# Kernel tuning notes

Hardware: AMD Instinct MI355X
Metric: run time of the kernel (lower is better)

## Reference

```python
import jax, jax.numpy as jnp
import numpy as np

D_MODEL = 1024
D_KEY = 64
N_HEADS = 16
B, T = 4, 2048


def setup_inputs() -> dict:
    key = jax.random.key(0)
    ks = jax.random.split(key, 12)
    s = 0.02
    return {
        "keys": jax.random.normal(ks[0], (B, T, D_MODEL), jnp.float32),
        "queries": jax.random.normal(ks[1], (B, T, D_MODEL), jnp.float32),
        "values": jax.random.normal(ks[2], (B, T, D_MODEL), jnp.float32),
        "pad_mask": jnp.ones((B, T), jnp.int32),
        "WK_w": jax.random.normal(ks[3], (D_KEY * N_HEADS, D_MODEL), jnp.float32) * s,
        "WK_b": jnp.zeros((D_KEY * N_HEADS,), jnp.float32),
        "WQ_w": jax.random.normal(ks[4], (D_KEY * N_HEADS, D_MODEL), jnp.float32) * s,
        "WQ_b": jnp.zeros((D_KEY * N_HEADS,), jnp.float32),
        "WV_w": jax.random.normal(ks[5], (D_KEY * N_HEADS, D_MODEL), jnp.float32) * s,
        "WV_b": jnp.zeros((D_KEY * N_HEADS,), jnp.float32),
        "WO_w": jax.random.normal(ks[6], (D_MODEL, D_KEY * N_HEADS), jnp.float32) * s,
        "WO_b": jnp.zeros((D_MODEL,), jnp.float32),
    }


def reference(keys, queries, values, pad_mask, WK_w, WK_b, WQ_w, WQ_b, WV_w, WV_b, WO_w, WO_b):
    # NOTE: the original torch module calls masked_fill (non-inplace) and discards
    # the result, so neither the causal mask nor pad_mask has any effect. We
    # faithfully reproduce that: no masking. pad_mask is an unused constant.
    batch, time = keys.shape[:2]
    k = keys @ WK_w.T + WK_b      # [B,T,H*dk]
    q = queries @ WQ_w.T + WQ_b
    v = values @ WV_w.T + WV_b

    def split_heads(x):
        return x.reshape(batch, time, N_HEADS, D_KEY).transpose(0, 2, 1, 3)  # [B,H,T,dk]

    k, q, v = split_heads(k), split_heads(q), split_heads(v)
    # scores[t,s] = k_t . q_s / sqrt(d_key)  (K and Q swapped, as in source)
    scores = jnp.einsum("bhtd,bhsd->bhts", k, q) / jnp.sqrt(jnp.float32(D_KEY))
    attn = jax.nn.softmax(scores, axis=-1)             # [B,H,T,T]
    ctx = jnp.einsum("bhts,bhsd->bhtd", attn, v)       # [B,H,T,dk]
    ctx = ctx.transpose(0, 2, 1, 3).reshape(batch, time, N_HEADS * D_KEY)
    return ctx @ WO_w.T + WO_b
```

## Files before the change

kernel.cpp:

```cpp
#include <hip/hip_runtime.h>

typedef unsigned short u16;
typedef unsigned int u32;
typedef __attribute__((ext_vector_type(8))) short short8;
typedef __attribute__((ext_vector_type(4))) float f32x4;

__device__ __forceinline__ u16 f2bf(float f) {
    unsigned int u = __float_as_uint(f);
    u += 0x7fffu + ((u >> 16) & 1u);
    return (u16)(u >> 16);
}

__device__ __forceinline__ u32 pack_trunc(float a, float b) {
    return __builtin_amdgcn_perm(__float_as_uint(b), __float_as_uint(a), 0x07060302u);
}

__device__ __forceinline__ void gload16(const u16* g, const u16* l) {
    __builtin_amdgcn_global_load_lds(
        (const __attribute__((address_space(1))) unsigned int*)g,
        (__attribute__((address_space(3))) unsigned int*)l, 16, 0, 0);
}

__global__ __launch_bounds__(256) void cast_all(const float* __restrict__ k,
                                                const float* __restrict__ q,
                                                const float* __restrict__ v,
                                                const float* __restrict__ wk,
                                                const float* __restrict__ wq,
                                                const float* __restrict__ wv,
                                                const float* __restrict__ wo,
                                                u16* __restrict__ Xk, u16* __restrict__ Xq,
                                                u16* __restrict__ Xv, u16* __restrict__ Wk,
                                                u16* __restrict__ Wq, u16* __restrict__ Wv,
                                                u16* __restrict__ Wo) {
    size_t i = ((size_t)blockIdx.x * 256 + threadIdx.x) * 8;
    const float* src; u16* dst; size_t off;
    if (i < 25165824) {
        int r = (int)(i >> 23); off = i & 8388607;
        src = r == 0 ? k : (r == 1 ? q : v);
        dst = r == 0 ? Xk : (r == 1 ? Xq : Xv);
    } else {
        size_t j = i - 25165824;
        int r = (int)(j >> 20); off = j & 1048575;
        src = r == 0 ? wk : (r == 1 ? wq : (r == 2 ? wv : wo));
        dst = r == 0 ? Wk : (r == 1 ? Wq : (r == 2 ? Wv : Wo));
    }
    float4 a = *(const float4*)(src + off);
    float4 b = *(const float4*)(src + off + 4);
    union { u16 h[8]; uint4 u; } r8;
    r8.h[0] = f2bf(a.x); r8.h[1] = f2bf(a.y); r8.h[2] = f2bf(a.z); r8.h[3] = f2bf(a.w);
    r8.h[4] = f2bf(b.x); r8.h[5] = f2bf(b.y); r8.h[6] = f2bf(b.z); r8.h[7] = f2bf(b.w);
    *(uint4*)(dst + off) = r8.u;
}

__global__ __launch_bounds__(256) void gemm_qkv(const u16* __restrict__ Xk,
                                                const u16* __restrict__ Xq,
                                                const u16* __restrict__ Xv,
                                                const u16* __restrict__ Wk,
                                                const u16* __restrict__ Wq,
                                                const u16* __restrict__ Wv,
                                                const float* __restrict__ bK,
                                                const float* __restrict__ bQ,
                                                const float* __restrict__ bV,
                                                u16* __restrict__ Kbh,
                                                u16* __restrict__ Qbh,
                                                u16* __restrict__ Vtg,
                                                float kscale) {
    __shared__ u16 sA[128 * 32];
    __shared__ u16 sB[128 * 32];
    const int f = blockIdx.x;
    const int z = f >> 9;
    const int r9 = f & 511;
    const int i_idx = (r9 & 7) | (((r9 >> 6) & 7) << 3);
    const int j_idx = (r9 >> 3) & 7;

    const u16* X = z == 0 ? Xk : (z == 1 ? Xq : Xv);
    const u16* W = z == 0 ? Wk : (z == 1 ? Wq : Wv);
    const float* bias = z == 0 ? bK : (z == 1 ? bQ : bV);
    u16* out = z == 0 ? Kbh : (z == 1 ? Qbh : Vtg);
    const float scale = z == 0 ? kscale : 1.0f;

    const int tid  = threadIdx.x;
    const int wave = tid >> 6, lane = tid & 63;
    const int quad = lane >> 4, l16 = lane & 15;
    const int wm = wave & 1, wn = wave >> 1;
    const int i0 = i_idx * 128, j0 = j_idx * 128;
    const int lrow = tid >> 2, lseg = tid & 3;

    f32x4 acc[4][4];
    #pragma unroll
    for (int mt = 0; mt < 4; mt++)
        #pragma unroll
        for (int nt = 0; nt < 4; nt++) acc[mt][nt] = (f32x4){0.f, 0.f, 0.f, 0.f};

    const u16* gA0 = X + (size_t)(i0 + lrow) * 1024 + lseg * 8;
    const u16* gA1 = X + (size_t)(i0 + 64 + lrow) * 1024 + lseg * 8;
    const u16* gB0 = W + (size_t)(j0 + lrow) * 1024 + lseg * 8;
    const u16* gB1 = W + (size_t)(j0 + 64 + lrow) * 1024 + lseg * 8;
    const u16* lA0 = sA + wave * 512;
    const u16* lA1 = sA + 2048 + wave * 512;
    const u16* lB0 = sB + wave * 512;
    const u16* lB1 = sB + 2048 + wave * 512;

    for (int kk = 0; kk < 1024; kk += 32) {
        __syncthreads();
        gload16(gA0 + kk, lA0);
        gload16(gA1 + kk, lA1);
        gload16(gB0 + kk, lB0);
        gload16(gB1 + kk, lB1);
        __syncthreads();
        short8 af[4], bf[4];
        #pragma unroll
        for (int mt = 0; mt < 4; mt++)
            af[mt] = *(const short8*)&sA[(wm * 64 + mt * 16 + l16) * 32 + quad * 8];
        #pragma unroll
        for (int nt = 0; nt < 4; nt++)
            bf[nt] = *(const short8*)&sB[(wn * 64 + nt * 16 + l16) * 32 + quad * 8];
        #pragma unroll
        for (int mt = 0; mt < 4; mt++)
            #pragma unroll
            for (int nt = 0; nt < 4; nt++)
                acc[mt][nt] = __builtin_amdgcn_mfma_f32_16x16x32_bf16(af[mt], bf[nt], acc[mt][nt], 0, 0, 0);
    }

    #pragma unroll
    for (int mt = 0; mt < 4; mt++) {
        #pragma unroll
        for (int nt = 0; nt < 4; nt++) {
            int j = j0 + wn * 64 + nt * 16 + l16;
            float bj = bias[j];
            #pragma unroll
            for (int r = 0; r < 4; r++) {
                int i = i0 + wm * 64 + mt * 16 + quad * 4 + r;
                float v = (acc[mt][nt][r] + bj) * scale;
                int b = i >> 11, t = i & 2047;
                int h = j >> 6,  dd = j & 63;
                size_t idx;
                if (z == 2) idx = (((size_t)(b * 16 + h)) * 64 + dd) * 2048 + t;
                else        idx = (((size_t)(b * 16 + h)) * 2048 + t) * 64 + dd;
                out[idx] = f2bf(v);
            }
        }
    }
}

__global__ __launch_bounds__(256) void gemm_out(const u16* __restrict__ X,
                                                const u16* __restrict__ W,
                                                const float* __restrict__ bias,
                                                float* __restrict__ out) {
    __shared__ u16 sA[128 * 32];
    __shared__ u16 sB[64 * 32];
    const int f = blockIdx.x;
    const int j_idx = (f >> 3) & 15;
    const int i_idx = (f & 7) | ((f >> 7) << 3);
    const int tid  = threadIdx.x;
    const int wave = tid >> 6, lane = tid & 63;
    const int quad = lane >> 4, l16 = lane & 15;
    const int wm = wave & 1, wn = wave >> 1;
    const int i0 = i_idx * 128, j0 = j_idx * 64;
    const int lrow = tid >> 2, lseg = tid & 3;

    f32x4 acc[4][2];
    #pragma unroll
    for (int mt = 0; mt < 4; mt++) {
        acc[mt][0] = (f32x4){0.f, 0.f, 0.f, 0.f};
        acc[mt][1] = (f32x4){0.f, 0.f, 0.f, 0.f};
    }

    const u16* gA0 = X + (size_t)(i0 + lrow) * 1024 + lseg * 8;
    const u16* gA1 = X + (size_t)(i0 + 64 + lrow) * 1024 + lseg * 8;
    const u16* gB0 = W + (size_t)(j0 + lrow) * 1024 + lseg * 8;
    const u16* lA0 = sA + wave * 512;
    const u16* lA1 = sA + 2048 + wave * 512;
    const u16* lB0 = sB + wave * 512;

    for (int kk = 0; kk < 1024; kk += 32) {
        __syncthreads();
        gload16(gA0 + kk, lA0);
        gload16(gA1 + kk, lA1);
        gload16(gB0 + kk, lB0);
        __syncthreads();
        short8 af[4], bf[2];
        #pragma unroll
        for (int mt = 0; mt < 4; mt++)
            af[mt] = *(const short8*)&sA[(wm * 64 + mt * 16 + l16) * 32 + quad * 8];
        #pragma unroll
        for (int nt = 0; nt < 2; nt++)
            bf[nt] = *(const short8*)&sB[(wn * 32 + nt * 16 + l16) * 32 + quad * 8];
        #pragma unroll
        for (int mt = 0; mt < 4; mt++)
            #pragma unroll
            for (int nt = 0; nt < 2; nt++)
                acc[mt][nt] = __builtin_amdgcn_mfma_f32_16x16x32_bf16(af[mt], bf[nt], acc[mt][nt], 0, 0, 0);
    }

    #pragma unroll
    for (int mt = 0; mt < 4; mt++) {
        #pragma unroll
        for (int nt = 0; nt < 2; nt++) {
            int j = j0 + wn * 32 + nt * 16 + l16;
            float bj = bias[j];
            #pragma unroll
            for (int r = 0; r < 4; r++) {
                int i = i0 + wm * 64 + mt * 16 + quad * 4 + r;
                out[(size_t)i * 1024 + j] = acc[mt][nt][r] + bj;
            }
        }
    }
}

#define QST 72

__global__ __launch_bounds__(256, 2) void attn_kernel(const u16* __restrict__ Kbh,
                                                      const u16* __restrict__ Qbh,
                                                      const u16* __restrict__ Vtg,
                                                      u16* __restrict__ ctx) {
    __shared__ u16 sQ[64 * QST];
    __shared__ u16 sVt[64 * QST];
    __shared__ u16 sP[4 * 2 * 16 * QST];
    const int f = blockIdx.x;
    const int bh = (f & 7) | ((f >> 6) << 3);
    const int tx = (f >> 3) & 7;
    const int tid  = threadIdx.x;
    const int wave = tid >> 6, lane = tid & 63;
    const int quad = lane >> 4, l16 = lane & 15;
    const int t0 = tx * 256;
    const int tw = t0 + wave * 64;
    const size_t base = (size_t)bh * 2048 * 64;

    short8 bk[4][2];
    #pragma unroll
    for (int g = 0; g < 4; g++) {
        const u16* kr = Kbh + base + (size_t)(tw + g * 16 + l16) * 64 + quad * 8;
        bk[g][0] = *(const short8*)kr;
        bk[g][1] = *(const short8*)(kr + 32);
    }
    const short8 ones = {0x3F80, 0x3F80, 0x3F80, 0x3F80, 0x3F80, 0x3F80, 0x3F80, 0x3F80};

    f32x4 accO[4][4];
    #pragma unroll
    for (int g = 0; g < 4; g++)
        #pragma unroll
        for (int dt = 0; dt < 4; dt++) accO[g][dt] = (f32x4){0.f, 0.f, 0.f, 0.f};
    f32x4 accL[4];
    #pragma unroll
    for (int g = 0; g < 4; g++) accL[g] = (f32x4){0.f, 0.f, 0.f, 0.f};

    const int srow = tid >> 2, seg = tid & 3;
    u16* sPw = sP + wave * 2 * 16 * QST;

    for (int s0 = 0; s0 < 2048; s0 += 64) {
        __syncthreads();
        {
            const uint4* gq = (const uint4*)(Qbh + base + (size_t)(s0 + srow) * 64 + seg * 16);
            uint4 q0 = gq[0], q1 = gq[1];
            *(uint4*)&sQ[srow * QST + seg * 16]     = q0;
            *(uint4*)&sQ[srow * QST + seg * 16 + 8] = q1;
        }
        {
            const uint4* gv = (const uint4*)(Vtg + ((size_t)bh * 64 + srow) * 2048 + s0 + seg * 16);
            uint4 v0 = gv[0], v1 = gv[1];
            *(uint4*)&sVt[srow * QST + seg * 16]     = v0;
            *(uint4*)&sVt[srow * QST + seg * 16 + 8] = v1;
        }
        __syncthreads();

        short8 aq[4][2], av[2][4];
        #pragma unroll
        for (int nt = 0; nt < 4; nt++) {
            aq[nt][0] = *(const short8*)&sQ[(nt * 16 + l16) * QST + quad * 8];
            aq[nt][1] = *(const short8*)&sQ[(nt * 16 + l16) * QST + 32 + quad * 8];
        }
        #pragma unroll
        for (int kk = 0; kk < 2; kk++)
            #pragma unroll
            for (int dt = 0; dt < 4; dt++)
                av[kk][dt] = *(const short8*)&sVt[(dt * 16 + l16) * QST + kk * 32 + quad * 8];

        #pragma unroll
        for (int g = 0; g < 4; g++) {
            f32x4 aS[4];
            #pragma unroll
            for (int nt = 0; nt < 4; nt++) {
                f32x4 s = __builtin_amdgcn_mfma_f32_16x16x32_bf16(aq[nt][0], bk[g][0],
                            (f32x4){0.f, 0.f, 0.f, 0.f}, 0, 0, 0);
                aS[nt] = __builtin_amdgcn_mfma_f32_16x16x32_bf16(aq[nt][1], bk[g][1], s, 0, 0, 0);
            }
            u16* pb = sPw + (g & 1) * 16 * QST;
            #pragma unroll
            for (int nt = 0; nt < 4; nt++) {
                float p0 = __builtin_amdgcn_exp2f(aS[nt][0]);
                float p1 = __builtin_amdgcn_exp2f(aS[nt][1]);
                float p2 = __builtin_amdgcn_exp2f(aS[nt][2]);
                float p3 = __builtin_amdgcn_exp2f(aS[nt][3]);
                uint2 pk = { pack_trunc(p0, p1), pack_trunc(p2, p3) };
                *(uint2*)&pb[l16 * QST + nt * 16 + quad * 4] = pk;
            }
            #pragma unroll
            for (int kk = 0; kk < 2; kk++) {
                short8 bp = *(const short8*)&pb[l16 * QST + kk * 32 + quad * 8];
                accL[g] = __builtin_amdgcn_mfma_f32_16x16x32_bf16(ones, bp, accL[g], 0, 0, 0);
                #pragma unroll
                for (int dt = 0; dt < 4; dt++)
                    accO[g][dt] = __builtin_amdgcn_mfma_f32_16x16x32_bf16(av[kk][dt], bp, accO[g][dt], 0, 0, 0);
            }
        }
    }

    const int b = bh >> 4, h = bh & 15;
    #pragma unroll
    for (int g = 0; g < 4; g++) {
        float inv = 1.f / accL[g][0];
        int t = tw + g * 16 + l16;
        u16* orow = ctx + ((size_t)(b * 2048 + t)) * 1024 + h * 64;
        #pragma unroll
        for (int dt = 0; dt < 4; dt++) {
            union { u16 h4[4]; uint2 u; } o;
            #pragma unroll
            for (int r = 0; r < 4; r++) o.h4[r] = f2bf(accO[g][dt][r] * inv);
            *(uint2*)&orow[dt * 16 + quad * 4] = o.u;
        }
    }
}

extern "C" void kernel_launch(void* const* d_in, const int* in_sizes, int n_in,
                              void* d_out, int out_size, void* d_ws, size_t ws_size,
                              hipStream_t stream) {
    const float* keys    = (const float*)d_in[0];
    const float* queries = (const float*)d_in[1];
    const float* values  = (const float*)d_in[2];
    const float* WKb = (const float*)d_in[5];
    const float* WQb = (const float*)d_in[7];
    const float* WVb = (const float*)d_in[9];
    const float* WOb = (const float*)d_in[11];

    char* ws = (char*)d_ws;
    const size_t MB = 1 << 20;
    u16* Kbh = (u16*)(ws + 0 * MB);
    u16* Qbh = (u16*)(ws + 16 * MB);
    u16* Vtg = (u16*)(ws + 32 * MB);
    u16* Xk  = (u16*)(ws + 48 * MB);
    u16* Xq  = (u16*)(ws + 64 * MB);
    u16* Xv  = (u16*)(ws + 80 * MB);
    u16* Wk  = (u16*)(ws + 96 * MB);
    u16* Wq  = (u16*)(ws + 98 * MB);
    u16* Wv  = (u16*)(ws + 100 * MB);
    u16* Wo  = (u16*)(ws + 102 * MB);
    u16* ctx = (u16*)(ws + 48 * MB);

    cast_all<<<14336, 256, 0, stream>>>(keys, queries, values,
                                        (const float*)d_in[4], (const float*)d_in[6],
                                        (const float*)d_in[8], (const float*)d_in[10],
                                        Xk, Xq, Xv, Wk, Wq, Wv, Wo);

    const float kscale = 1.4426950408889634f * 0.125f;
    gemm_qkv<<<1536, 256, 0, stream>>>(Xk, Xq, Xv, Wk, Wq, Wv,
                                       WKb, WQb, WVb, Kbh, Qbh, Vtg, kscale);

    attn_kernel<<<512, 256, 0, stream>>>(Kbh, Qbh, Vtg, ctx);

    gemm_out<<<1024, 256, 0, stream>>>(ctx, Wo, WOb, (float*)d_out);
}
```

Measured before the change: 346.4 us.

## Double-buffer LDS tiles and swizzle layout in projection GEMMs

Both projection GEMM kernels now use two LDS buffers, so the next k-slice is loaded while the current one feeds MFMA. This removes one of the two barriers per iteration. The 16-byte chunk position within each LDS row is also XOR-swizzled by row bits, with matching swizzled reads, to reduce bank conflicts on fragment loads. LDS use doubles, which may lower occupancy, and overlap depends on how the compiler places the waitcnt before the barrier.

```diff
diff --git a/kernel.cpp b/kernel.cpp
--- a/kernel.cpp
+++ b/kernel.cpp
@@ -65,8 +65,8 @@
                                                 u16* __restrict__ Qbh,
                                                 u16* __restrict__ Vtg,
                                                 float kscale) {
-    __shared__ u16 sA[128 * 32];
-    __shared__ u16 sB[128 * 32];
+    __shared__ u16 sA[2 * 128 * 32];
+    __shared__ u16 sB[2 * 128 * 32];
     const int f = blockIdx.x;
     const int z = f >> 9;
     const int r9 = f & 511;
@@ -84,7 +84,9 @@
     const int quad = lane >> 4, l16 = lane & 15;
     const int wm = wave & 1, wn = wave >> 1;
     const int i0 = i_idx * 128, j0 = j_idx * 128;
-    const int lrow = tid >> 2, lseg = tid & 3;
+    const int lrow = tid >> 2;
+    const int lseg = (tid & 3) ^ ((tid >> 3) & 3);
+    const int sw   = (l16 >> 1) & 3;
 
     f32x4 acc[4][4];
     #pragma unroll
@@ -96,30 +98,38 @@
     const u16* gA1 = X + (size_t)(i0 + 64 + lrow) * 1024 + lseg * 8;
     const u16* gB0 = W + (size_t)(j0 + lrow) * 1024 + lseg * 8;
     const u16* gB1 = W + (size_t)(j0 + 64 + lrow) * 1024 + lseg * 8;
-    const u16* lA0 = sA + wave * 512;
-    const u16* lA1 = sA + 2048 + wave * 512;
-    const u16* lB0 = sB + wave * 512;
-    const u16* lB1 = sB + 2048 + wave * 512;
+
+    auto stage = [&](int buf, int kk) {
+        const u16* a = sA + buf * 4096 + wave * 512;
+        const u16* b = sB + buf * 4096 + wave * 512;
+        gload16(gA0 + kk, a);
+        gload16(gA1 + kk, a + 2048);
+        gload16(gB0 + kk, b);
+        gload16(gB1 + kk, b + 2048);
+    };
+
+    stage(0, 0);
+    __syncthreads();
+    int cur = 0;
 
     for (int kk = 0; kk < 1024; kk += 32) {
-        __syncthreads();
-        gload16(gA0 + kk, lA0);
-        gload16(gA1 + kk, lA1);
-        gload16(gB0 + kk, lB0);
-        gload16(gB1 + kk, lB1);
-        __syncthreads();
+        if (kk + 32 < 1024) stage(cur ^ 1, kk + 32);
+        const u16* bA = sA + cur * 4096;
+        const u16* bB = sB + cur * 4096;
         short8 af[4], bf[4];
         #pragma unroll
         for (int mt = 0; mt < 4; mt++)
-            af[mt] = *(const short8*)&sA[(wm * 64 + mt * 16 + l16) * 32 + quad * 8];
+            af[mt] = *(const short8*)&bA[(wm * 64 + mt * 16 + l16) * 32 + (quad ^ sw) * 8];
         #pragma unroll
         for (int nt = 0; nt < 4; nt++)
-            bf[nt] = *(const short8*)&sB[(wn * 64 + nt * 16 + l16) * 32 + quad * 8];
+            bf[nt] = *(const short8*)&bB[(wn * 64 + nt * 16 + l16) * 32 + (quad ^ sw) * 8];
         #pragma unroll
         for (int mt = 0; mt < 4; mt++)
             #pragma unroll
             for (int nt = 0; nt < 4; nt++)
                 acc[mt][nt] = __builtin_amdgcn_mfma_f32_16x16x32_bf16(af[mt], bf[nt], acc[mt][nt], 0, 0, 0);
+        __syncthreads();
+        cur ^= 1;
     }
 
     #pragma unroll
@@ -147,8 +157,8 @@
                                                 const u16* __restrict__ W,
                                                 const float* __restrict__ bias,
                                                 float* __restrict__ out) {
-    __shared__ u16 sA[128 * 32];
-    __shared__ u16 sB[64 * 32];
+    __shared__ u16 sA[2 * 128 * 32];
+    __shared__ u16 sB[2 * 64 * 32];
     const int f = blockIdx.x;
     const int j_idx = (f >> 3) & 15;
     const int i_idx = (f & 7) | ((f >> 7) << 3);
@@ -157,7 +167,9 @@
     const int quad = lane >> 4, l16 = lane & 15;
     const int wm = wave & 1, wn = wave >> 1;
     const int i0 = i_idx * 128, j0 = j_idx * 64;
-    const int lrow = tid >> 2, lseg = tid & 3;
+    const int lrow = tid >> 2;
+    const int lseg = (tid & 3) ^ ((tid >> 3) & 3);
+    const int sw   = (l16 >> 1) & 3;
 
     f32x4 acc[4][2];
     #pragma unroll
@@ -169,28 +181,37 @@
     const u16* gA0 = X + (size_t)(i0 + lrow) * 1024 + lseg * 8;
     const u16* gA1 = X + (size_t)(i0 + 64 + lrow) * 1024 + lseg * 8;
     const u16* gB0 = W + (size_t)(j0 + lrow) * 1024 + lseg * 8;
-    const u16* lA0 = sA + wave * 512;
-    const u16* lA1 = sA + 2048 + wave * 512;
-    const u16* lB0 = sB + wave * 512;
+
+    auto stage = [&](int buf, int kk) {
+        const u16* a = sA + buf * 4096 + wave * 512;
+        const u16* b = sB + buf * 2048 + wave * 512;
+        gload16(gA0 + kk, a);
+        gload16(gA1 + kk, a + 2048);
+        gload16(gB0 + kk, b);
+    };
+
+    stage(0, 0);
+    __syncthreads();
+    int cur = 0;
 
     for (int kk = 0; kk < 1024; kk += 32) {
-        __syncthreads();
-        gload16(gA0 + kk, lA0);
-        gload16(gA1 + kk, lA1);
-        gload16(gB0 + kk, lB0);
-        __syncthreads();
+        if (kk + 32 < 1024) stage(cur ^ 1, kk + 32);
+        const u16* bA = sA + cur * 4096;
+        const u16* bB = sB + cur * 2048;
         short8 af[4], bf[2];
         #pragma unroll
         for (int mt = 0; mt < 4; mt++)
-            af[mt] = *(const short8*)&sA[(wm * 64 + mt * 16 + l16) * 32 + quad * 8];
+            af[mt] = *(const short8*)&bA[(wm * 64 + mt * 16 + l16) * 32 + (quad ^ sw) * 8];
         #pragma unroll
         for (int nt = 0; nt < 2; nt++)
-            bf[nt] = *(const short8*)&sB[(wn * 32 + nt * 16 + l16) * 32 + quad * 8];
+            bf[nt] = *(const short8*)&bB[(wn * 32 + nt * 16 + l16) * 32 + (quad ^ sw) * 8];
         #pragma unroll
         for (int mt = 0; mt < 4; mt++)
             #pragma unroll
             for (int nt = 0; nt < 2; nt++)
                 acc[mt][nt] = __builtin_amdgcn_mfma_f32_16x16x32_bf16(af[mt], bf[nt], acc[mt][nt], 0, 0, 0);
+        __syncthreads();
+        cur ^= 1;
     }
 
     #pragma unroll
```

Result: slower. 362.6 us (+4.7%).

## Rewrite projection GEMMs with 256x128 tiles, triple-buffered LDS and swizzle

Applied to the files above, without the earlier changes.

Both the QKV and output projection GEMMs now use 512-thread blocks computing 256x128 tiles with a K-step of 64. A three-stage LDS ring (144 KB of dynamic shared memory) lets global-to-LDS loads for future tiles overlap MFMA work, and an XOR swizzle on the LDS layout avoids bank conflicts. The block index remapping is meant to improve L2 locality. In exchange, LDS use is high enough to limit occupancy, and gemm_out launches only 256 blocks, which may underfill the GPU's compute units.

```diff
diff --git a/kernel.cpp b/kernel.cpp
--- a/kernel.cpp
+++ b/kernel.cpp
@@ -52,26 +52,107 @@
     *(uint4*)(dst + off) = r8.u;
 }
 
-__global__ __launch_bounds__(256) void gemm_qkv(const u16* __restrict__ Xk,
-                                                const u16* __restrict__ Xq,
-                                                const u16* __restrict__ Xv,
-                                                const u16* __restrict__ Wk,
-                                                const u16* __restrict__ Wq,
-                                                const u16* __restrict__ Wv,
-                                                const float* __restrict__ bK,
-                                                const float* __restrict__ bQ,
-                                                const float* __restrict__ bV,
-                                                u16* __restrict__ Kbh,
-                                                u16* __restrict__ Qbh,
-                                                u16* __restrict__ Vtg,
-                                                float kscale) {
-    __shared__ u16 sA[128 * 32];
-    __shared__ u16 sB[128 * 32];
-    const int f = blockIdx.x;
-    const int z = f >> 9;
-    const int r9 = f & 511;
-    const int i_idx = (r9 & 7) | (((r9 >> 6) & 7) << 3);
-    const int j_idx = (r9 >> 3) & 7;
+
+__device__ __forceinline__ void stage_tile(const u16* __restrict__ X, const u16* __restrict__ W,
+                                           int i0, int j0, int kt, u16* sA, u16* sB,
+                                           int tid, int wave) {
+    const int r = tid >> 3;
+    const int sg = (tid & 7) ^ (r & 7);
+    const u16* gA = X + (size_t)(i0 + r) * 1024 + kt + sg * 8;
+    const u16* gB = W + (size_t)(j0 + r) * 1024 + kt + sg * 8;
+    const u16* dA = sA + wave * 512;
+    const u16* dB = sB + wave * 512;
+    gload16(gA,               dA);
+    gload16(gA + 64 * 1024,   dA + 4096);
+    gload16(gA + 128 * 1024,  dA + 8192);
+    gload16(gA + 192 * 1024,  dA + 12288);
+    gload16(gB,               dB);
+    gload16(gB + 64 * 1024,   dB + 4096);
+}
+
+__device__ __forceinline__ void tile_mfma(const u16* sA, const u16* sB,
+                                          f32x4 (&acc)[8][2],
+                                          int wm, int wn, int quad, int l16) {
+    const int sx = l16 & 7;
+    short8 bf[2][2];
+    #pragma unroll
+    for (int nf = 0; nf < 2; nf++)
+        #pragma unroll
+        for (int kh = 0; kh < 2; kh++) {
+            int row = wn * 32 + nf * 16 + l16;
+            int slot = (quad + kh * 4) ^ sx;
+            bf[nf][kh] = *(const short8*)&sB[row * 64 + slot * 8];
+        }
+    #pragma unroll
+    for (int mh = 0; mh < 2; mh++) {
+        short8 af[4][2];
+        #pragma unroll
+        for (int mf = 0; mf < 4; mf++)
+            #pragma unroll
+            for (int kh = 0; kh < 2; kh++) {
+                int row = wm * 128 + mh * 64 + mf * 16 + l16;
+                int slot = (quad + kh * 4) ^ sx;
+                af[mf][kh] = *(const short8*)&sA[row * 64 + slot * 8];
+            }
+        #pragma unroll
+        for (int mf = 0; mf < 4; mf++)
+            #pragma unroll
+            for (int nf = 0; nf < 2; nf++)
+                #pragma unroll
+                for (int kh = 0; kh < 2; kh++)
+                    acc[mh * 4 + mf][nf] = __builtin_amdgcn_mfma_f32_16x16x32_bf16(
+                        af[mf][kh], bf[nf][kh], acc[mh * 4 + mf][nf], 0, 0, 0);
+    }
+}
+
+#define GEMM_PIPELINE(X, W)                                                              \
+    stage_tile(X, W, i0, j0, 0,  sAr,         sBr,        tid, wave);                    \
+    stage_tile(X, W, i0, j0, 64, sAr + 16384, sBr + 8192, tid, wave);                    \
+    int rs = 0;                                                                          \
+    _Pragma("unroll 1")                                                                  \
+    for (int t = 0; t < 14; t++) {                                                       \
+        asm volatile("s_waitcnt vmcnt(6)" ::: "memory");                                 \
+        __builtin_amdgcn_s_barrier();                                                    \
+        __builtin_amdgcn_s_setprio(1);                                                   \
+        tile_mfma(sAr + rs * 16384, sBr + rs * 8192, acc, wm, wn, quad, l16);            \
+        __builtin_amdgcn_s_setprio(0);                                                   \
+        __builtin_amdgcn_s_barrier();                                                    \
+        int ss = rs + 2; if (ss >= 3) ss -= 3;                                           \
+        stage_tile(X, W, i0, j0, (t + 2) * 64, sAr + ss * 16384, sBr + ss * 8192,        \
+                   tid, wave);                                                           \
+        rs = (rs == 2) ? 0 : rs + 1;                                                     \
+    }                                                                                    \
+    asm volatile("s_waitcnt vmcnt(6)" ::: "memory");             \
+    __builtin_amdgcn_s_barrier();                                                        \
+    tile_mfma(sAr + rs * 16384, sBr + rs * 8192, acc, wm, wn, quad, l16);                \
+    __builtin_amdgcn_s_barrier();                                                        \
+    rs = (rs == 2) ? 0 : rs + 1;                                                         \
+    asm volatile("s_waitcnt vmcnt(0)" ::: "memory");                     \
+    __builtin_amdgcn_s_barrier();                                                        \
+    tile_mfma(sAr + rs * 16384, sBr + rs * 8192, acc, wm, wn, quad, l16);
+
+__global__ __launch_bounds__(512, 2) void gemm_qkv(const u16* __restrict__ Xk,
+                                                   const u16* __restrict__ Xq,
+                                                   const u16* __restrict__ Xv,
+                                                   const u16* __restrict__ Wk,
+                                                   const u16* __restrict__ Wq,
+                                                   const u16* __restrict__ Wv,
+                                                   const float* __restrict__ bK,
+                                                   const float* __restrict__ bQ,
+                                                   const float* __restrict__ bV,
+                                                   u16* __restrict__ Kbh,
+                                                   u16* __restrict__ Qbh,
+                                                   u16* __restrict__ Vtg,
+                                                   float kscale) {
+    extern __shared__ __align__(16) u16 smem[];
+    u16* sAr = smem;
+    u16* sBr = smem + 49152;
+    const int f  = blockIdx.x;
+    const int wg = (f & 7) * 96 + (f >> 3);
+    const int z  = wg >> 8;
+    const int r8 = wg & 255;
+    const int i0 = (r8 >> 3) * 256;
+    const int j0 = (r8 & 7) * 128;
 
     const u16* X = z == 0 ? Xk : (z == 1 ? Xq : Xv);
     const u16* W = z == 0 ? Wk : (z == 1 ? Wq : Wv);
@@ -82,127 +163,74 @@
     const int tid  = threadIdx.x;
     const int wave = tid >> 6, lane = tid & 63;
     const int quad = lane >> 4, l16 = lane & 15;
-    const int wm = wave & 1, wn = wave >> 1;
-    const int i0 = i_idx * 128, j0 = j_idx * 128;
-    const int lrow = tid >> 2, lseg = tid & 3;
-
-    f32x4 acc[4][4];
-    #pragma unroll
-    for (int mt = 0; mt < 4; mt++)
-        #pragma unroll
-        for (int nt = 0; nt < 4; nt++) acc[mt][nt] = (f32x4){0.f, 0.f, 0.f, 0.f};
-
-    const u16* gA0 = X + (size_t)(i0 + lrow) * 1024 + lseg * 8;
-    const u16* gA1 = X + (size_t)(i0 + 64 + lrow) * 1024 + lseg * 8;
-    const u16* gB0 = W + (size_t)(j0 + lrow) * 1024 + lseg * 8;
-    const u16* gB1 = W + (size_t)(j0 + 64 + lrow) * 1024 + lseg * 8;
-    const u16* lA0 = sA + wave * 512;
-    const u16* lA1 = sA + 2048 + wave * 512;
-    const u16* lB0 = sB + wave * 512;
-    const u16* lB1 = sB + 2048 + wave * 512;
-
-    for (int kk = 0; kk < 1024; kk += 32) {
-        __syncthreads();
-        gload16(gA0 + kk, lA0);
-        gload16(gA1 + kk, lA1);
-        gload16(gB0 + kk, lB0);
-        gload16(gB1 + kk, lB1);
-        __syncthreads();
-        short8 af[4], bf[4];
-        #pragma unroll
-        for (int mt = 0; mt < 4; mt++)
-            af[mt] = *(const short8*)&sA[(wm * 64 + mt * 16 + l16) * 32 + quad * 8];
-        #pragma unroll
-        for (int nt = 0; nt < 4; nt++)
-            bf[nt] = *(const short8*)&sB[(wn * 64 + nt * 16 + l16) * 32 + quad * 8];
-        #pragma unroll
-        for (int mt = 0; mt < 4; mt++)
-            #pragma unroll
-            for (int nt = 0; nt < 4; nt++)
-                acc[mt][nt] = __builtin_amdgcn_mfma_f32_16x16x32_bf16(af[mt], bf[nt], acc[mt][nt], 0, 0, 0);
-    }
-
-    #pragma unroll
-    for (int mt = 0; mt < 4; mt++) {
-        #pragma unroll
-        for (int nt = 0; nt < 4; nt++) {
-            int j = j0 + wn * 64 + nt * 16 + l16;
+    const int wm = wave >> 2, wn = wave & 3;
+
+    f32x4 acc[8][2];
+    #pragma unroll
+    for (int m = 0; m < 8; m++) {
+        acc[m][0] = (f32x4){0.f, 0.f, 0.f, 0.f};
+        acc[m][1] = (f32x4){0.f, 0.f, 0.f, 0.f};
+    }
+
+    GEMM_PIPELINE(X, W)
+
+    #pragma unroll
+    for (int m = 0; m < 8; m++) {
+        #pragma unroll
+        for (int nf = 0; nf < 2; nf++) {
+            int j = j0 + wn * 32 + nf * 16 + l16;
             float bj = bias[j];
             #pragma unroll
             for (int r = 0; r < 4; r++) {
-                int i = i0 + wm * 64 + mt * 16 + quad * 4 + r;
-                float v = (acc[mt][nt][r] + bj) * scale;
-                int b = i >> 11, t = i & 2047;
+                int i = i0 + wm * 128 + m * 16 + quad * 4 + r;
+                float v = (acc[m][nf][r] + bj) * scale;
+                int b = i >> 11, tt = i & 2047;
                 int h = j >> 6,  dd = j & 63;
                 size_t idx;
-                if (z == 2) idx = (((size_t)(b * 16 + h)) * 64 + dd) * 2048 + t;
-                else        idx = (((size_t)(b * 16 + h)) * 2048 + t) * 64 + dd;
+                if (z == 2) idx = (((size_t)(b * 16 + h)) * 64 + dd) * 2048 + tt;
+                else        idx = (((size_t)(b * 16 + h)) * 2048 + tt) * 64 + dd;
                 out[idx] = f2bf(v);
             }
         }
     }
 }
 
-__global__ __launch_bounds__(256) void gemm_out(const u16* __restrict__ X,
-                                                const u16* __restrict__ W,
-                                                const float* __restrict__ bias,
-                                                float* __restrict__ out) {
-    __shared__ u16 sA[128 * 32];
-    __shared__ u16 sB[64 * 32];
-    const int f = blockIdx.x;
-    const int j_idx = (f >> 3) & 15;
-    const int i_idx = (f & 7) | ((f >> 7) << 3);
+__global__ __launch_bounds__(512, 2) void gemm_out(const u16* __restrict__ X,
+                                                   const u16* __restrict__ W,
+                                                   const float* __restrict__ bias,
+                                                   float* __restrict__ out) {
+    extern __shared__ __align__(16) u16 smem[];
+    u16* sAr = smem;
+    u16* sBr = smem + 49152;
+    const int f  = blockIdx.x;
+    const int wg = (f & 7) * 32 + (f >> 3);
+    const int i0 = (wg >> 3) * 256;
+    const int j0 = (wg & 7) * 128;
+
     const int tid  = threadIdx.x;
     const int wave = tid >> 6, lane = tid & 63;
     const int quad = lane >> 4, l16 = lane & 15;
-    const int wm = wave & 1, wn = wave >> 1;
-    const int i0 = i_idx * 128, j0 = j_idx * 64;
-    const int lrow = tid >> 2, lseg = tid & 3;
-
-    f32x4 acc[4][2];
-    #pragma unroll
-    for (int mt = 0; mt < 4; mt++) {
-        acc[mt][0] = (f32x4){0.f, 0.f, 0.f, 0.f};
-        acc[mt][1] = (f32x4){0.f, 0.f, 0.f, 0.f};
-    }
-
-    const u16* gA0 = X + (size_t)(i0 + lrow) * 1024 + lseg * 8;
-    const u16* gA1 = X + (size_t)(i0 + 64 + lrow) * 1024 + lseg * 8;
-    const u16* gB0 = W + (size_t)(j0 + lrow) * 1024 + lseg * 8;
-    const u16* lA0 = sA + wave * 512;
-    const u16* lA1 = sA + 2048 + wave * 512;
-    const u16* lB0 = sB + wave * 512;
-
-    for (int kk = 0; kk < 1024; kk += 32) {
-        __syncthreads();
-        gload16(gA0 + kk, lA0);
-        gload16(gA1 + kk, lA1);
-        gload16(gB0 + kk, lB0);
-        __syncthreads();
-        short8 af[4], bf[2];
-        #pragma unroll
-        for (int mt = 0; mt < 4; mt++)
-            af[mt] = *(const short8*)&sA[(wm * 64 + mt * 16 + l16) * 32 + quad * 8];
-        #pragma unroll
-        for (int nt = 0; nt < 2; nt++)
-            bf[nt] = *(const short8*)&sB[(wn * 32 + nt * 16 + l16) * 32 + quad * 8];
-        #pragma unroll
-        for (int mt = 0; mt < 4; mt++)
-            #pragma unroll
-            for (int nt = 0; nt < 2; nt++)
-                acc[mt][nt] = __builtin_amdgcn_mfma_f32_16x16x32_bf16(af[mt], bf[nt], acc[mt][nt], 0, 0, 0);
-    }
-
-    #pragma unroll
-    for (int mt = 0; mt < 4; mt++) {
-        #pragma unroll
-        for (int nt = 0; nt < 2; nt++) {
-            int j = j0 + wn * 32 + nt * 16 + l16;
+    const int wm = wave >> 2, wn = wave & 3;
+
+    f32x4 acc[8][2];
+    #pragma unroll
+    for (int m = 0; m < 8; m++) {
+        acc[m][0] = (f32x4){0.f, 0.f, 0.f, 0.f};
+        acc[m][1] = (f32x4){0.f, 0.f, 0.f, 0.f};
+    }
+
+    GEMM_PIPELINE(X, W)
+
+    #pragma unroll
+    for (int m = 0; m < 8; m++) {
+        #pragma unroll
+        for (int nf = 0; nf < 2; nf++) {
+            int j = j0 + wn * 32 + nf * 16 + l16;
             float bj = bias[j];
             #pragma unroll
             for (int r = 0; r < 4; r++) {
-                int i = i0 + wm * 64 + mt * 16 + quad * 4 + r;
-                out[(size_t)i * 1024 + j] = acc[mt][nt][r] + bj;
+                int i = i0 + wm * 128 + m * 16 + quad * 4 + r;
+                out[(size_t)i * 1024 + j] = acc[m][nf][r] + bj;
             }
         }
     }
@@ -347,16 +375,25 @@
     u16* Wo  = (u16*)(ws + 102 * MB);
     u16* ctx = (u16*)(ws + 48 * MB);
 
+    static bool attr_done = false;
+    if (!attr_done) {
+        hipFuncSetAttribute((const void*)gemm_qkv,
+                            hipFuncAttributeMaxDynamicSharedMemorySize, 147456);
+        hipFuncSetAttribute((const void*)gemm_out,
+                            hipFuncAttributeMaxDynamicSharedMemorySize, 147456);
+        attr_done = true;
+    }
+
     cast_all<<<14336, 256, 0, stream>>>(keys, queries, values,
                                         (const float*)d_in[4], (const float*)d_in[6],
                                         (const float*)d_in[8], (const float*)d_in[10],
                                         Xk, Xq, Xv, Wk, Wq, Wv, Wo);
 
     const float kscale = 1.4426950408889634f * 0.125f;
-    gemm_qkv<<<1536, 256, 0, stream>>>(Xk, Xq, Xv, Wk, Wq, Wv,
-                                       WKb, WQb, WVb, Kbh, Qbh, Vtg, kscale);
+    gemm_qkv<<<768, 512, 147456, stream>>>(Xk, Xq, Xv, Wk, Wq, Wv,
+                                           WKb, WQb, WVb, Kbh, Qbh, Vtg, kscale);
 
     attn_kernel<<<512, 256, 0, stream>>>(Kbh, Qbh, Vtg, ctx);
 
-    gemm_out<<<1024, 256, 0, stream>>>(ctx, Wo, WOb, (float*)d_out);
-}
+    gemm_out<<<256, 512, 147456, stream>>>(ctx, Wo, WOb, (float*)d_out);
+}
```

Measured after the change: 358.3 us. +3.4%, slower.

## Double GEMM K-tile to 64 and XOR-swizzle LDS layout in projection kernels

Applied to the files above, without the earlier changes.

Both the QKV and output projection GEMMs now stage a 64-wide K slice per iteration instead of 32, halving the number of barrier pairs and load rounds across the K loop. The LDS tile is stored with an XOR swizzle on 16-byte segments (applied on the global source side, since global_load_lds writes contiguously), so fragment reads from 64-element rows avoid bank conflicts. This doubles LDS use per block, which may reduce occupancy, and there is still no double buffering.

```diff
diff --git a/kernel.cpp b/kernel.cpp
--- a/kernel.cpp
+++ b/kernel.cpp
@@ -52,6 +52,7 @@
     *(uint4*)(dst + off) = r8.u;
 }
 
+
 __global__ __launch_bounds__(256) void gemm_qkv(const u16* __restrict__ Xk,
                                                 const u16* __restrict__ Xq,
                                                 const u16* __restrict__ Xv,
@@ -65,8 +66,8 @@
                                                 u16* __restrict__ Qbh,
                                                 u16* __restrict__ Vtg,
                                                 float kscale) {
-    __shared__ u16 sA[128 * 32];
-    __shared__ u16 sB[128 * 32];
+    __shared__ u16 sA[128 * 64];
+    __shared__ u16 sB[128 * 64];
     const int f = blockIdx.x;
     const int z = f >> 9;
     const int r9 = f & 511;
@@ -84,7 +85,14 @@
     const int quad = lane >> 4, l16 = lane & 15;
     const int wm = wave & 1, wn = wave >> 1;
     const int i0 = i_idx * 128, j0 = j_idx * 128;
-    const int lrow = tid >> 2, lseg = tid & 3;
+
+    const int r = tid >> 3;
+    const int sg = (tid & 7) ^ (r & 7);
+    const u16* gA = X + (size_t)(i0 + r) * 1024 + sg * 8;
+    const u16* gB = W + (size_t)(j0 + r) * 1024 + sg * 8;
+    u16* dA = sA + wave * 512;
+    u16* dB = sB + wave * 512;
+    const int sx = l16 & 7;
 
     f32x4 acc[4][4];
     #pragma unroll
@@ -92,34 +100,35 @@
         #pragma unroll
         for (int nt = 0; nt < 4; nt++) acc[mt][nt] = (f32x4){0.f, 0.f, 0.f, 0.f};
 
-    const u16* gA0 = X + (size_t)(i0 + lrow) * 1024 + lseg * 8;
-    const u16* gA1 = X + (size_t)(i0 + 64 + lrow) * 1024 + lseg * 8;
-    const u16* gB0 = W + (size_t)(j0 + lrow) * 1024 + lseg * 8;
-    const u16* gB1 = W + (size_t)(j0 + 64 + lrow) * 1024 + lseg * 8;
-    const u16* lA0 = sA + wave * 512;
-    const u16* lA1 = sA + 2048 + wave * 512;
-    const u16* lB0 = sB + wave * 512;
-    const u16* lB1 = sB + 2048 + wave * 512;
-
-    for (int kk = 0; kk < 1024; kk += 32) {
-        __syncthreads();
-        gload16(gA0 + kk, lA0);
-        gload16(gA1 + kk, lA1);
-        gload16(gB0 + kk, lB0);
-        gload16(gB1 + kk, lB1);
-        __syncthreads();
-        short8 af[4], bf[4];
-        #pragma unroll
-        for (int mt = 0; mt < 4; mt++)
-            af[mt] = *(const short8*)&sA[(wm * 64 + mt * 16 + l16) * 32 + quad * 8];
+    for (int kk = 0; kk < 1024; kk += 64) {
+        __syncthreads();
+        gload16(gA + kk,         dA);
+        gload16(gA + kk + 32768, dA + 2048);
+        gload16(gA + kk + 65536, dA + 4096);
+        gload16(gA + kk + 98304, dA + 6144);
+        gload16(gB + kk,         dB);
+        gload16(gB + kk + 32768, dB + 2048);
+        gload16(gB + kk + 65536, dB + 4096);
+        gload16(gB + kk + 98304, dB + 6144);
+        __syncthreads();
+        short8 bf[4][2];
         #pragma unroll
         for (int nt = 0; nt < 4; nt++)
-            bf[nt] = *(const short8*)&sB[(wn * 64 + nt * 16 + l16) * 32 + quad * 8];
-        #pragma unroll
-        for (int mt = 0; mt < 4; mt++)
-            #pragma unroll
-            for (int nt = 0; nt < 4; nt++)
-                acc[mt][nt] = __builtin_amdgcn_mfma_f32_16x16x32_bf16(af[mt], bf[nt], acc[mt][nt], 0, 0, 0);
+            #pragma unroll
+            for (int kh = 0; kh < 2; kh++)
+                bf[nt][kh] = *(const short8*)&sB[(wn * 64 + nt * 16 + l16) * 64 +
+                                                 ((kh * 4 + quad) ^ sx) * 8];
+        #pragma unroll
+        for (int mt = 0; mt < 4; mt++) {
+            const int arow = (wm * 64 + mt * 16 + l16) * 64;
+            short8 a0 = *(const short8*)&sA[arow + ((quad) ^ sx) * 8];
+            short8 a1 = *(const short8*)&sA[arow + ((4 + quad) ^ sx) * 8];
+            #pragma unroll
+            for (int nt = 0; nt < 4; nt++) {
+                acc[mt][nt] = __builtin_amdgcn_mfma_f32_16x16x32_bf16(a0, bf[nt][0], acc[mt][nt], 0, 0, 0);
+                acc[mt][nt] = __builtin_amdgcn_mfma_f32_16x16x32_bf16(a1, bf[nt][1], acc[mt][nt], 0, 0, 0);
+            }
+        }
     }
 
     #pragma unroll
@@ -129,9 +138,9 @@
             int j = j0 + wn * 64 + nt * 16 + l16;
             float bj = bias[j];
             #pragma unroll
-            for (int r = 0; r < 4; r++) {
-                int i = i0 + wm * 64 + mt * 16 + quad * 4 + r;
-                float v = (acc[mt][nt][r] + bj) * scale;
+            for (int rr = 0; rr < 4; rr++) {
+                int i = i0 + wm * 64 + mt * 16 + quad * 4 + rr;
+                float v = (acc[mt][nt][rr] + bj) * scale;
                 int b = i >> 11, t = i & 2047;
                 int h = j >> 6,  dd = j & 63;
                 size_t idx;
@@ -147,8 +156,8 @@
                                                 const u16* __restrict__ W,
                                                 const float* __restrict__ bias,
                                                 float* __restrict__ out) {
-    __shared__ u16 sA[128 * 32];
-    __shared__ u16 sB[64 * 32];
+    __shared__ u16 sA[128 * 64];
+    __shared__ u16 sB[64 * 64];
     const int f = blockIdx.x;
     const int j_idx = (f >> 3) & 15;
     const int i_idx = (f & 7) | ((f >> 7) << 3);
@@ -157,7 +166,14 @@
     const int quad = lane >> 4, l16 = lane & 15;
     const int wm = wave & 1, wn = wave >> 1;
     const int i0 = i_idx * 128, j0 = j_idx * 64;
-    const int lrow = tid >> 2, lseg = tid & 3;
+
+    const int r = tid >> 3;
+    const int sg = (tid & 7) ^ (r & 7);
+    const u16* gA = X + (size_t)(i0 + r) * 1024 + sg * 8;
+    const u16* gB = W + (size_t)(j0 + r) * 1024 + sg * 8;
+    u16* dA = sA + wave * 512;
+    u16* dB = sB + wave * 512;
+    const int sx = l16 & 7;
 
     f32x4 acc[4][2];
     #pragma unroll
@@ -166,31 +182,33 @@
         acc[mt][1] = (f32x4){0.f, 0.f, 0.f, 0.f};
     }
 
-    const u16* gA0 = X + (size_t)(i0 + lrow) * 1024 + lseg * 8;
-    const u16* gA1 = X + (size_t)(i0 + 64 + lrow) * 1024 + lseg * 8;
-    const u16* gB0 = W + (size_t)(j0 + lrow) * 1024 + lseg * 8;
-    const u16* lA0 = sA + wave * 512;
-    const u16* lA1 = sA + 2048 + wave * 512;
-    const u16* lB0 = sB + wave * 512;
-
-    for (int kk = 0; kk < 1024; kk += 32) {
-        __syncthreads();
-        gload16(gA0 + kk, lA0);
-        gload16(gA1 + kk, lA1);
-        gload16(gB0 + kk, lB0);
-        __syncthreads();
-        short8 af[4], bf[2];
-        #pragma unroll
-        for (int mt = 0; mt < 4; mt++)
-            af[mt] = *(const short8*)&sA[(wm * 64 + mt * 16 + l16) * 32 + quad * 8];
+    for (int kk = 0; kk < 1024; kk += 64) {
+        __syncthreads();
+        gload16(gA + kk,         dA);
+        gload16(gA + kk + 32768, dA + 2048);
+        gload16(gA + kk + 65536, dA + 4096);
+        gload16(gA + kk + 98304, dA + 6144);
+        gload16(gB + kk,         dB);
+        gload16(gB + kk + 32768, dB + 2048);
+        __syncthreads();
+        short8 bf[2][2];
         #pragma unroll
         for (int nt = 0; nt < 2; nt++)
-            bf[nt] = *(const short8*)&sB[(wn * 32 + nt * 16 + l16) * 32 + quad * 8];
-        #pragma unroll
-        for (int mt = 0; mt < 4; mt++)
-            #pragma unroll
-            for (int nt = 0; nt < 2; nt++)
-                acc[mt][nt] = __builtin_amdgcn_mfma_f32_16x16x32_bf16(af[mt], bf[nt], acc[mt][nt], 0, 0, 0);
+            #pragma unroll
+            for (int kh = 0; kh < 2; kh++)
+                bf[nt][kh] = *(const short8*)&sB[(wn * 32 + nt * 16 + l16) * 64 +
+                                                 ((kh * 4 + quad) ^ sx) * 8];
+        #pragma unroll
+        for (int mt = 0; mt < 4; mt++) {
+            const int arow = (wm * 64 + mt * 16 + l16) * 64;
+            short8 a0 = *(const short8*)&sA[arow + ((quad) ^ sx) * 8];
+            short8 a1 = *(const short8*)&sA[arow + ((4 + quad) ^ sx) * 8];
+            #pragma unroll
+            for (int nt = 0; nt < 2; nt++) {
+                acc[mt][nt] = __builtin_amdgcn_mfma_f32_16x16x32_bf16(a0, bf[nt][0], acc[mt][nt], 0, 0, 0);
+                acc[mt][nt] = __builtin_amdgcn_mfma_f32_16x16x32_bf16(a1, bf[nt][1], acc[mt][nt], 0, 0, 0);
+            }
+        }
     }
 
     #pragma unroll
@@ -200,9 +218,9 @@
             int j = j0 + wn * 32 + nt * 16 + l16;
             float bj = bias[j];
             #pragma unroll
-            for (int r = 0; r < 4; r++) {
-                int i = i0 + wm * 64 + mt * 16 + quad * 4 + r;
-                out[(size_t)i * 1024 + j] = acc[mt][nt][r] + bj;
+            for (int rr = 0; rr < 4; rr++) {
+                int i = i0 + wm * 64 + mt * 16 + quad * 4 + rr;
+                out[(size_t)i * 1024 + j] = acc[mt][nt][rr] + bj;
             }
         }
     }
@@ -316,7 +334,7 @@
         for (int dt = 0; dt < 4; dt++) {
             union { u16 h4[4]; uint2 u; } o;
             #pragma unroll
-            for (int r = 0; r < 4; r++) o.h4[r] = f2bf(accO[g][dt][r] * inv);
+            for (int rr = 0; rr < 4; rr++) o.h4[rr] = f2bf(accO[g][dt][rr] * inv);
             *(uint2*)&orow[dt * 16 + quad * 4] = o.u;
         }
     }
```

Result: faster. 334.9 us (-3.3%).
